# Performance work log

Hardware: AMD Instinct MI355X
Metric: run time of the kernel (lower is better)

The kernel has to match this reference:

```python
import jax, jax.numpy as jnp
import numpy as np

N = 8192
C_IN = 128
C_OUT = 128


def setup_inputs() -> dict:
    key = jax.random.key(0)
    k1, k2, k3, k4 = jax.random.split(key, 4)
    x = jax.random.normal(k1, (N, C_IN), dtype=jnp.float32)
    adj = jax.random.uniform(k2, (N, N), dtype=jnp.float32)
    mask = jax.random.uniform(k3, (N, N), dtype=jnp.float32)
    # nn.Linear(c_in, c_out, bias=False) weight has shape [c_out, c_in]
    W = jax.random.normal(k4, (C_OUT, C_IN), dtype=jnp.float32) * (1.0 / np.sqrt(C_IN))
    return {"x": x, "adj": adj, "mask": mask, "W": W}


def reference(x, adj, mask, W):
    n = adj.shape[0]
    # adj = adj * mask + I  (mask application plus self-loops)
    adj_eff = adj * mask + jnp.eye(n, dtype=adj.dtype)
    # h = x @ W^T  (Linear, no bias), then aggregate: out = adj_eff @ h
    h = jnp.einsum("nc,oc->no", x, W)  # [N, c_out]
    return jnp.matmul(adj_eff, h)       # [N, c_out]
```

## Files before the change

### kernel.cpp

```cpp
#include <hip/hip_runtime.h>
#include <hip/hip_bf16.h>
#include <stdint.h>

#define NROW 8192
#define CD 128
#define SPLITK 8
#define KCHUNK (NROW / SPLITK)
#define BK 64
#define NITER (KCHUNK / BK)

typedef __bf16 bf16_t;
typedef __bf16 bf16x8 __attribute__((ext_vector_type(8)));
typedef __bf16 bf16x4 __attribute__((ext_vector_type(4)));
typedef float f32x4 __attribute__((ext_vector_type(4)));

__device__ __forceinline__ f32x4 mfma16(bf16x8 a, bf16x8 b, f32x4 c) {
    return __builtin_amdgcn_mfma_f32_16x16x32_bf16(a, b, c, 0, 0, 0);
}

__device__ __forceinline__ void dma16(const void* g, void* l) {
    __builtin_amdgcn_global_load_lds(
        (const __attribute__((address_space(1))) uint32_t*)g,
        (__attribute__((address_space(3))) uint32_t*)l, 16, 0, 0);
}

__device__ __forceinline__ bf16x8 load_cvt_bf16(const float* __restrict__ p) {
    float4 a0 = *(const float4*)p;
    float4 a1 = *(const float4*)(p + 4);
    bf16x8 r;
    r[0] = (bf16_t)a0.x; r[1] = (bf16_t)a0.y; r[2] = (bf16_t)a0.z; r[3] = (bf16_t)a0.w;
    r[4] = (bf16_t)a1.x; r[5] = (bf16_t)a1.y; r[6] = (bf16_t)a1.z; r[7] = (bf16_t)a1.w;
    return r;
}

__global__ __launch_bounds__(256)
void h_kernel(const float* __restrict__ x, const float* __restrict__ W,
              bf16_t* __restrict__ hT, float* __restrict__ out)
{
    __shared__ __align__(16) float h_sl_all[4][16 * 128];
    const int tid = threadIdx.x;
    const int w = tid >> 6, lane = tid & 63;
    const int m = lane & 15, q = lane >> 4;
    const int rb = blockIdx.x * 64 + w * 16;

    f32x4 acc[8] = {};
#pragma unroll
    for (int k0 = 0; k0 < CD; k0 += 32) {
        bf16x8 af = load_cvt_bf16(x + (size_t)(rb + m) * CD + k0 + q * 8);
#pragma unroll
        for (int c = 0; c < 8; ++c) {
            bf16x8 bv = load_cvt_bf16(W + (size_t)(c * 16 + m) * CD + k0 + q * 8);
            acc[c] = mfma16(af, bv, acc[c]);
        }
    }
    float* hs = h_sl_all[w];
#pragma unroll
    for (int c = 0; c < 8; ++c)
#pragma unroll
        for (int j = 0; j < 4; ++j)
            hs[(q * 4 + j) * 128 + c * 16 + m] = acc[c][j];

    float* dst = out + (size_t)rb * CD;
#pragma unroll
    for (int t = 0; t < 8; ++t) {
        int fi = t * 64 + lane;
        *(float4*)(dst + fi * 4) = *(const float4*)(hs + fi * 4);
    }
#pragma unroll
    for (int t = 0; t < 4; ++t) {
        int idx = t * 64 + lane;
        int c = idx >> 1, nc = idx & 1;
        bf16x8 v;
#pragma unroll
        for (int j = 0; j < 8; ++j)
            v[j] = (bf16_t)hs[(nc * 8 + j) * 128 + c];
        *(bf16x8*)(hT + (size_t)c * NROW + rb + nc * 8) = v;
    }
}

template <bool ATOMIC>
__global__ __launch_bounds__(256)
void gemm_kernel(const float* __restrict__ adj, const float* __restrict__ mask,
                 const bf16_t* __restrict__ hT, float* __restrict__ outp)
{
    __shared__ __align__(16) ushort lds_all[32768];
    ushort* const Ab0 = lds_all;
    ushort* const Ab1 = lds_all + 8192;
    ushort* const Bb0 = lds_all + 16384;
    ushort* const Bb1 = lds_all + 24576;

    const int tid  = threadIdx.x;
    const int w    = tid >> 6;
    const int lane = tid & 63;
    const int m = lane & 15;
    const int q = lane >> 4;
    const int rowbase = blockIdx.x * 128;
    const int kbeg = blockIdx.y * KCHUNK;

    f32x4 acc[2][8] = {};
    float4 va[8], vm[8];

    auto loadA = [&](int it) {
        const int kw = kbeg + it * BK;
#pragma unroll
        for (int rr = 0; rr < 8; ++rr) {
            int idx = rr * 256 + tid;
            int row = idx >> 4, c4 = idx & 15;
            va[rr] = *(const float4*)(adj  + (size_t)(rowbase + row) * NROW + kw + c4 * 4);
            vm[rr] = *(const float4*)(mask + (size_t)(rowbase + row) * NROW + kw + c4 * 4);
        }
    };
    auto dmaB = [&](int it, ushort* Bb) {
        const int kw = kbeg + it * BK;
#pragma unroll
        for (int rr = 0; rr < 4; ++rr) {
            int P = w * 256 + rr * 64 + lane;
            int row = P >> 3;
            int pc = (P & 7) ^ (row & 7);
            dma16(hT + (size_t)row * NROW + kw + pc * 8, Bb + (size_t)P * 8);
        }
    };
    auto storeA = [&](ushort* Abuf) {
#pragma unroll
        for (int rr = 0; rr < 8; ++rr) {
            int idx = rr * 256 + tid;
            int row = idx >> 4, c4 = idx & 15;
            int sw = (c4 >> 1) ^ (row & 7);
            bf16x4 v;
            v[0] = (bf16_t)(va[rr].x * vm[rr].x);
            v[1] = (bf16_t)(va[rr].y * vm[rr].y);
            v[2] = (bf16_t)(va[rr].z * vm[rr].z);
            v[3] = (bf16_t)(va[rr].w * vm[rr].w);
            *(bf16x4*)(Abuf + row * 64 + sw * 8 + (c4 & 1) * 4) = v;
        }
    };
    auto compute = [&](const ushort* Abuf, const ushort* Bbuf) {
#pragma unroll
        for (int ss = 0; ss < 2; ++ss) {
            const int pc = ss * 4 + q;
            const int sw = pc ^ (m & 7);
            bf16x8 af[2];
#pragma unroll
            for (int r = 0; r < 2; ++r) {
                int row = w * 32 + r * 16 + m;
                af[r] = *(const bf16x8*)(Abuf + row * 64 + sw * 8);
            }
#pragma unroll
            for (int c = 0; c < 8; ++c) {
                int row = c * 16 + m;
                bf16x8 bv = *(const bf16x8*)(Bbuf + row * 64 + sw * 8);
#pragma unroll
                for (int r = 0; r < 2; ++r)
                    acc[r][c] = mfma16(af[r], bv, acc[r][c]);
            }
        }
    };

    loadA(0);
    dmaB(0, Bb0);
    storeA(Ab0);

    for (int it = 0; it < NITER; ++it) {
        __syncthreads();
        const bool nx = (it + 1) < NITER;
        ushort* An = (it & 1) ? Ab0 : Ab1;
        ushort* Bn = (it & 1) ? Bb0 : Bb1;
        const ushort* Ac = (it & 1) ? Ab1 : Ab0;
        const ushort* Bc = (it & 1) ? Bb1 : Bb0;
        if (nx) { loadA(it + 1); dmaB(it + 1, Bn); }
        compute(Ac, Bc);
        if (nx) storeA(An);
    }

    __syncthreads();
    float* h_sl = (float*)lds_all + w * 4096;
#pragma unroll
    for (int r = 0; r < 2; ++r)
#pragma unroll
        for (int c = 0; c < 8; ++c)
#pragma unroll
            for (int j = 0; j < 4; ++j)
                h_sl[(r * 16 + q * 4 + j) * 128 + c * 16 + m] = acc[r][c][j];

    if (!ATOMIC) {
        float* dst = outp + (size_t)blockIdx.y * ((size_t)NROW * CD)
                   + (size_t)(rowbase + w * 32) * CD;
#pragma unroll
        for (int t = 0; t < 16; ++t) {
            int fi = t * 64 + lane;
            *(float4*)(dst + fi * 4) = *(const float4*)(h_sl + fi * 4);
        }
    } else {
        float* dst = outp + (size_t)(rowbase + w * 32) * CD;
        for (int t = 0; t < 64; ++t) {
            int ei = t * 64 + lane;
            atomicAdd(dst + ei, h_sl[ei]);
        }
    }
}

__global__ void reduce_kernel(float* __restrict__ out, const float* __restrict__ part)
{
    const size_t i = ((size_t)blockIdx.x * 256 + threadIdx.x) * 4;
    float4 sum = *(const float4*)(out + i);
#pragma unroll
    for (int sp = 0; sp < SPLITK; ++sp) {
        float4 p = *(const float4*)(part + (size_t)sp * ((size_t)NROW * CD) + i);
        sum.x += p.x; sum.y += p.y; sum.z += p.z; sum.w += p.w;
    }
    *(float4*)(out + i) = sum;
}

extern "C" void kernel_launch(void* const* d_in, const int* in_sizes, int n_in,
                              void* d_out, int out_size, void* d_ws, size_t ws_size,
                              hipStream_t stream)
{
    const float* x    = (const float*)d_in[0];
    const float* adj  = (const float*)d_in[1];
    const float* mask = (const float*)d_in[2];
    const float* W    = (const float*)d_in[3];
    float* out = (float*)d_out;

    bf16_t* hT = (bf16_t*)d_ws;
    const size_t HT_BYTES   = (size_t)CD * NROW * sizeof(bf16_t);
    const size_t PART_BYTES = (size_t)SPLITK * NROW * CD * sizeof(float);

    h_kernel<<<dim3(NROW / 64), dim3(256), 0, stream>>>(x, W, hT, out);

    if (ws_size >= HT_BYTES + PART_BYTES) {
        float* part = (float*)((char*)d_ws + HT_BYTES);
        gemm_kernel<false><<<dim3(64, SPLITK), dim3(256), 0, stream>>>(adj, mask, hT, part);
        reduce_kernel<<<dim3(1024), dim3(256), 0, stream>>>(out, part);
    } else {
        gemm_kernel<true><<<dim3(64, SPLITK), dim3(256), 0, stream>>>(adj, mask, hT, out);
    }
}
```

Before: 573.7 us.

## Replace LDS-staged GEMM with register-direct streaming loads and more blocks

Rewrites the aggregation GEMM so each wave reads its own adj/mask rows and hT fragments straight from global memory into registers, with nontemporal loads and software double-buffering. This removes LDS staging, swizzling and block barriers. Each block now covers 64 rows instead of 128, so the grid grows from 512 to 1024 blocks. hT reads are no longer shared through LDS across waves and rely on cache reuse instead. The h kernel shrinks to single-wave blocks, and outputs are written straight from the accumulators with nontemporal stores.

```diff
diff --git a/kernel.cpp b/kernel.cpp
--- a/kernel.cpp
+++ b/kernel.cpp
@@ -6,42 +6,33 @@
 #define CD 128
 #define SPLITK 8
 #define KCHUNK (NROW / SPLITK)
-#define BK 64
-#define NITER (KCHUNK / BK)
+#define KSTEPS (KCHUNK / 32)
 
 typedef __bf16 bf16_t;
 typedef __bf16 bf16x8 __attribute__((ext_vector_type(8)));
-typedef __bf16 bf16x4 __attribute__((ext_vector_type(4)));
 typedef float f32x4 __attribute__((ext_vector_type(4)));
 
 __device__ __forceinline__ f32x4 mfma16(bf16x8 a, bf16x8 b, f32x4 c) {
     return __builtin_amdgcn_mfma_f32_16x16x32_bf16(a, b, c, 0, 0, 0);
 }
 
-__device__ __forceinline__ void dma16(const void* g, void* l) {
-    __builtin_amdgcn_global_load_lds(
-        (const __attribute__((address_space(1))) uint32_t*)g,
-        (__attribute__((address_space(3))) uint32_t*)l, 16, 0, 0);
-}
-
 __device__ __forceinline__ bf16x8 load_cvt_bf16(const float* __restrict__ p) {
-    float4 a0 = *(const float4*)p;
-    float4 a1 = *(const float4*)(p + 4);
+    f32x4 a0 = *(const f32x4*)p;
+    f32x4 a1 = *(const f32x4*)(p + 4);
     bf16x8 r;
     r[0] = (bf16_t)a0.x; r[1] = (bf16_t)a0.y; r[2] = (bf16_t)a0.z; r[3] = (bf16_t)a0.w;
     r[4] = (bf16_t)a1.x; r[5] = (bf16_t)a1.y; r[6] = (bf16_t)a1.z; r[7] = (bf16_t)a1.w;
     return r;
 }
 
-__global__ __launch_bounds__(256)
+__global__ __launch_bounds__(64)
 void h_kernel(const float* __restrict__ x, const float* __restrict__ W,
               bf16_t* __restrict__ hT, float* __restrict__ out)
 {
-    __shared__ __align__(16) float h_sl_all[4][16 * 128];
-    const int tid = threadIdx.x;
-    const int w = tid >> 6, lane = tid & 63;
+    __shared__ __align__(16) float hs[16 * 128];
+    const int lane = threadIdx.x;
     const int m = lane & 15, q = lane >> 4;
-    const int rb = blockIdx.x * 64 + w * 16;
+    const int rb = blockIdx.x * 16;
 
     f32x4 acc[8] = {};
 #pragma unroll
@@ -53,18 +44,18 @@
             acc[c] = mfma16(af, bv, acc[c]);
         }
     }
-    float* hs = h_sl_all[w];
 #pragma unroll
     for (int c = 0; c < 8; ++c)
 #pragma unroll
         for (int j = 0; j < 4; ++j)
             hs[(q * 4 + j) * 128 + c * 16 + m] = acc[c][j];
+    __syncthreads();
 
     float* dst = out + (size_t)rb * CD;
 #pragma unroll
     for (int t = 0; t < 8; ++t) {
         int fi = t * 64 + lane;
-        *(float4*)(dst + fi * 4) = *(const float4*)(hs + fi * 4);
+        *(f32x4*)(dst + fi * 4) = *(const f32x4*)(hs + fi * 4);
     }
 #pragma unroll
     for (int t = 0; t < 4; ++t) {
@@ -83,132 +74,95 @@
 void gemm_kernel(const float* __restrict__ adj, const float* __restrict__ mask,
                  const bf16_t* __restrict__ hT, float* __restrict__ outp)
 {
-    __shared__ __align__(16) ushort lds_all[32768];
-    ushort* const Ab0 = lds_all;
-    ushort* const Ab1 = lds_all + 8192;
-    ushort* const Bb0 = lds_all + 16384;
-    ushort* const Bb1 = lds_all + 24576;
-
     const int tid  = threadIdx.x;
     const int w    = tid >> 6;
     const int lane = tid & 63;
-    const int m = lane & 15;
-    const int q = lane >> 4;
-    const int rowbase = blockIdx.x * 128;
+    const int m = lane & 15, q = lane >> 4;
+    const int row  = blockIdx.x * 64 + w * 16 + m;
     const int kbeg = blockIdx.y * KCHUNK;
 
-    f32x4 acc[2][8] = {};
-    float4 va[8], vm[8];
+    const float*  pa = adj  + (size_t)row * NROW + kbeg + q * 8;
+    const float*  pm = mask + (size_t)row * NROW + kbeg + q * 8;
+    const bf16_t* pb = hT   + (size_t)m   * NROW + kbeg + q * 8;
 
-    auto loadA = [&](int it) {
-        const int kw = kbeg + it * BK;
+    f32x4 acc[8] = {};
+
+    f32x4 aA0, aA1, xA0, xA1, aB0, aB1, xB0, xB1;
+    bf16x8 bA[8], bB[8];
+
+    auto loadA = [&](int it, f32x4& a0, f32x4& a1, f32x4& x0, f32x4& x1) {
+        const float* p0 = pa + it * 32;
+        const float* p1 = pm + it * 32;
+        a0 = __builtin_nontemporal_load((const f32x4*)p0);
+        a1 = __builtin_nontemporal_load((const f32x4*)(p0 + 4));
+        x0 = __builtin_nontemporal_load((const f32x4*)p1);
+        x1 = __builtin_nontemporal_load((const f32x4*)(p1 + 4));
+    };
+    auto loadB = [&](int it, bf16x8* b) {
 #pragma unroll
-        for (int rr = 0; rr < 8; ++rr) {
-            int idx = rr * 256 + tid;
-            int row = idx >> 4, c4 = idx & 15;
-            va[rr] = *(const float4*)(adj  + (size_t)(rowbase + row) * NROW + kw + c4 * 4);
-            vm[rr] = *(const float4*)(mask + (size_t)(rowbase + row) * NROW + kw + c4 * 4);
-        }
+        for (int c = 0; c < 8; ++c)
+            b[c] = *(const bf16x8*)(pb + (size_t)c * 16 * NROW + it * 32);
     };
-    auto dmaB = [&](int it, ushort* Bb) {
-        const int kw = kbeg + it * BK;
+    auto comp = [&](const f32x4& a0, const f32x4& a1,
+                    const f32x4& x0, const f32x4& x1, const bf16x8* b) {
+        bf16x8 af;
+        af[0] = (bf16_t)(a0.x * x0.x);
+        af[1] = (bf16_t)(a0.y * x0.y);
+        af[2] = (bf16_t)(a0.z * x0.z);
+        af[3] = (bf16_t)(a0.w * x0.w);
+        af[4] = (bf16_t)(a1.x * x1.x);
+        af[5] = (bf16_t)(a1.y * x1.y);
+        af[6] = (bf16_t)(a1.z * x1.z);
+        af[7] = (bf16_t)(a1.w * x1.w);
 #pragma unroll
-        for (int rr = 0; rr < 4; ++rr) {
-            int P = w * 256 + rr * 64 + lane;
-            int row = P >> 3;
-            int pc = (P & 7) ^ (row & 7);
-            dma16(hT + (size_t)row * NROW + kw + pc * 8, Bb + (size_t)P * 8);
-        }
-    };
-    auto storeA = [&](ushort* Abuf) {
-#pragma unroll
-        for (int rr = 0; rr < 8; ++rr) {
-            int idx = rr * 256 + tid;
-            int row = idx >> 4, c4 = idx & 15;
-            int sw = (c4 >> 1) ^ (row & 7);
-            bf16x4 v;
-            v[0] = (bf16_t)(va[rr].x * vm[rr].x);
-            v[1] = (bf16_t)(va[rr].y * vm[rr].y);
-            v[2] = (bf16_t)(va[rr].z * vm[rr].z);
-            v[3] = (bf16_t)(va[rr].w * vm[rr].w);
-            *(bf16x4*)(Abuf + row * 64 + sw * 8 + (c4 & 1) * 4) = v;
-        }
-    };
-    auto compute = [&](const ushort* Abuf, const ushort* Bbuf) {
-#pragma unroll
-        for (int ss = 0; ss < 2; ++ss) {
-            const int pc = ss * 4 + q;
-            const int sw = pc ^ (m & 7);
-            bf16x8 af[2];
-#pragma unroll
-            for (int r = 0; r < 2; ++r) {
-                int row = w * 32 + r * 16 + m;
-                af[r] = *(const bf16x8*)(Abuf + row * 64 + sw * 8);
-            }
-#pragma unroll
-            for (int c = 0; c < 8; ++c) {
-                int row = c * 16 + m;
-                bf16x8 bv = *(const bf16x8*)(Bbuf + row * 64 + sw * 8);
-#pragma unroll
-                for (int r = 0; r < 2; ++r)
-                    acc[r][c] = mfma16(af[r], bv, acc[r][c]);
-            }
-        }
+        for (int c = 0; c < 8; ++c)
+            acc[c] = mfma16(af, b[c], acc[c]);
     };
 
-    loadA(0);
-    dmaB(0, Bb0);
-    storeA(Ab0);
-
-    for (int it = 0; it < NITER; ++it) {
-        __syncthreads();
-        const bool nx = (it + 1) < NITER;
-        ushort* An = (it & 1) ? Ab0 : Ab1;
-        ushort* Bn = (it & 1) ? Bb0 : Bb1;
-        const ushort* Ac = (it & 1) ? Ab1 : Ab0;
-        const ushort* Bc = (it & 1) ? Bb1 : Bb0;
-        if (nx) { loadA(it + 1); dmaB(it + 1, Bn); }
-        compute(Ac, Bc);
-        if (nx) storeA(An);
+    loadA(0, aA0, aA1, xA0, xA1);
+    loadB(0, bA);
+#pragma unroll
+    for (int it = 0; it < KSTEPS / 2; ++it) {
+        loadA(2 * it + 1, aB0, aB1, xB0, xB1);
+        loadB(2 * it + 1, bB);
+        comp(aA0, aA1, xA0, xA1, bA);
+        if (it + 1 < KSTEPS / 2) {
+            loadA(2 * it + 2, aA0, aA1, xA0, xA1);
+            loadB(2 * it + 2, bA);
+        }
+        comp(aB0, aB1, xB0, xB1, bB);
     }
 
-    __syncthreads();
-    float* h_sl = (float*)lds_all + w * 4096;
-#pragma unroll
-    for (int r = 0; r < 2; ++r)
+    if (!ATOMIC) {
+        float* dst = outp + (size_t)blockIdx.y * ((size_t)NROW * CD)
+                   + (size_t)(blockIdx.x * 64 + w * 16) * CD;
 #pragma unroll
         for (int c = 0; c < 8; ++c)
 #pragma unroll
             for (int j = 0; j < 4; ++j)
-                h_sl[(r * 16 + q * 4 + j) * 128 + c * 16 + m] = acc[r][c][j];
-
-    if (!ATOMIC) {
-        float* dst = outp + (size_t)blockIdx.y * ((size_t)NROW * CD)
-                   + (size_t)(rowbase + w * 32) * CD;
+                __builtin_nontemporal_store(acc[c][j],
+                    dst + (q * 4 + j) * CD + c * 16 + m);
+    } else {
+        float* dst = outp + (size_t)(blockIdx.x * 64 + w * 16) * CD;
 #pragma unroll
-        for (int t = 0; t < 16; ++t) {
-            int fi = t * 64 + lane;
-            *(float4*)(dst + fi * 4) = *(const float4*)(h_sl + fi * 4);
-        }
-    } else {
-        float* dst = outp + (size_t)(rowbase + w * 32) * CD;
-        for (int t = 0; t < 64; ++t) {
-            int ei = t * 64 + lane;
-            atomicAdd(dst + ei, h_sl[ei]);
-        }
+        for (int c = 0; c < 8; ++c)
+#pragma unroll
+            for (int j = 0; j < 4; ++j)
+                atomicAdd(dst + (q * 4 + j) * CD + c * 16 + m, acc[c][j]);
     }
 }
 
 __global__ void reduce_kernel(float* __restrict__ out, const float* __restrict__ part)
 {
     const size_t i = ((size_t)blockIdx.x * 256 + threadIdx.x) * 4;
-    float4 sum = *(const float4*)(out + i);
+    f32x4 sum = *(const f32x4*)(out + i);
 #pragma unroll
     for (int sp = 0; sp < SPLITK; ++sp) {
-        float4 p = *(const float4*)(part + (size_t)sp * ((size_t)NROW * CD) + i);
-        sum.x += p.x; sum.y += p.y; sum.z += p.z; sum.w += p.w;
+        f32x4 p = __builtin_nontemporal_load(
+            (const f32x4*)(part + (size_t)sp * ((size_t)NROW * CD) + i));
+        sum += p;
     }
-    *(float4*)(out + i) = sum;
+    *(f32x4*)(out + i) = sum;
 }
 
 extern "C" void kernel_launch(void* const* d_in, const int* in_sizes, int n_in,
@@ -225,13 +179,13 @@
     const size_t HT_BYTES   = (size_t)CD * NROW * sizeof(bf16_t);
     const size_t PART_BYTES = (size_t)SPLITK * NROW * CD * sizeof(float);
 
-    h_kernel<<<dim3(NROW / 64), dim3(256), 0, stream>>>(x, W, hT, out);
+    h_kernel<<<dim3(NROW / 16), dim3(64), 0, stream>>>(x, W, hT, out);
 
     if (ws_size >= HT_BYTES + PART_BYTES) {
         float* part = (float*)((char*)d_ws + HT_BYTES);
-        gemm_kernel<false><<<dim3(64, SPLITK), dim3(256), 0, stream>>>(adj, mask, hT, part);
+        gemm_kernel<false><<<dim3(NROW / 64, SPLITK), dim3(256), 0, stream>>>(adj, mask, hT, part);
         reduce_kernel<<<dim3(1024), dim3(256), 0, stream>>>(out, part);
     } else {
-        gemm_kernel<true><<<dim3(64, SPLITK), dim3(256), 0, stream>>>(adj, mask, hT, out);
+        gemm_kernel<true><<<dim3(NROW / 64, SPLITK), dim3(256), 0, stream>>>(adj, mask, hT, out);
     }
 }
```

Result: slower. 699.4 us (+21.9%).
